# Performance work log

Hardware: AMD Instinct MI355X
Metric: run time of the kernel (lower is better)

The kernel has to match this reference:

```python
import jax, jax.numpy as jnp
import numpy as np

B, N, E, D, H, HW, L = 16, 32, 256, 256, 8, 784, 4
DH = D // H
FF = 4 * D
BN = B * N
BE = B * E
SCALE = 1.0 / np.sqrt(DH)


def _ln(x, g, b):
    m = x.mean(-1, keepdims=True)
    v = ((x - m) ** 2).mean(-1, keepdims=True)
    return (x - m) * jax.lax.rsqrt(v + 1e-5) * g + b


def setup_inputs() -> dict:
    key = jax.random.key(0)
    ks = iter(jax.random.split(key, 64))
    def w(shape, s=0.05):
        return jax.random.normal(next(ks), shape, jnp.float32) * s
    inp = {
        'nodes': w((B, N, D), 1.0),
        'edges': w((B, E, D), 1.0),
        'images': w((B, HW, D), 1.0),
        'mask': jnp.zeros((B * H, N + E, HW), jnp.float32),
        'node_enc': w((BN, D), 1.0),
        'edge_enc': w((BE, D), 1.0),
        'ln1_g': jnp.ones((L, D), jnp.float32), 'ln1_b': jnp.zeros((L, D), jnp.float32),
        'Wqkv': w((L, D, 3 * D)), 'bqkv': jnp.zeros((L, 3 * D), jnp.float32),
        'Wo': w((L, D, D)), 'bo': jnp.zeros((L, D), jnp.float32),
        'ls1': jnp.full((L, D), 0.1, jnp.float32),
        'ln2_g': jnp.ones((L, D), jnp.float32), 'ln2_b': jnp.zeros((L, D), jnp.float32),
        'Wn1': w((L, D, D)), 'bn1': jnp.zeros((L, D), jnp.float32),
        'Wn2': w((L, D, D)), 'bn2': jnp.zeros((L, D), jnp.float32),
        'We': w((L, D, D)), 'be': jnp.zeros((L, D), jnp.float32),
        'attn_p': w((L, H, DH), 1.0),
        'Weo': w((L, D, D)), 'beo': jnp.zeros((L, D), jnp.float32),
        'Wno': w((L, D, D)), 'bno': jnp.zeros((L, D), jnp.float32),
        'ls2': jnp.full((L, D), 0.1, jnp.float32),
        'ln3_g': jnp.ones((L, D), jnp.float32), 'ln3_b': jnp.zeros((L, D), jnp.float32),
        'W1': w((L, D, FF)), 'b1': jnp.zeros((L, FF), jnp.float32),
        'W2': w((L, FF, D)), 'b2': jnp.zeros((L, D), jnp.float32),
        'ls3': jnp.full((L, D), 0.1, jnp.float32),
        'edge_index': jax.random.randint(next(ks), (2, BE), 0, BN, jnp.int32),
    }
    return inp


def reference(nodes, edges, images, mask, node_enc, edge_enc,
              ln1_g, ln1_b, Wqkv, bqkv, Wo, bo, ls1,
              ln2_g, ln2_b, Wn1, bn1, Wn2, bn2, We, be, attn_p, Weo, beo, Wno, bno, ls2,
              ln3_g, ln3_b, W1, b1, W2, b2, ls3, edge_index):
    idx0, idx1 = edge_index[0], edge_index[1]
    ne = jnp.concatenate([nodes, edges], axis=1)  # [B, N+E, D]
    mask4 = mask.reshape(B, H, N + E, HW)
    for l in range(L):
        # cross-attention ne -> images
        ne1n = _ln(ne, ln1_g[l], ln1_b[l])
        q = (ne1n @ Wqkv[l, :, :D] + bqkv[l, :D]).reshape(B, N + E, H, DH)
        k = (images @ Wqkv[l, :, D:2 * D] + bqkv[l, D:2 * D]).reshape(B, HW, H, DH)
        v = (images @ Wqkv[l, :, 2 * D:] + bqkv[l, 2 * D:]).reshape(B, HW, H, DH)
        scores = jnp.einsum('bqhd,bkhd->bhqk', q, k) * SCALE + mask4
        attn = jax.nn.softmax(scores, axis=-1)
        ctx = jnp.einsum('bhqk,bkhd->bqhd', attn, v).reshape(B, N + E, D)
        ne1 = ne + ls1[l] * (ctx @ Wo[l] + bo[l])
        # modified GAT on flattened graph
        ne2n = _ln(ne1, ln2_g[l], ln2_b[l])
        nodes_f = ne2n[:, :N].reshape(BN, D) + node_enc
        edges_f = ne2n[:, N:].reshape(BE, D) + edge_enc
        fn = (nodes_f @ Wn1[l] + bn1[l])[idx0]
        sn = (nodes_f @ Wn2[l] + bn2[l])[idx0]  # NOTE: original code uses edge_index[0] here too
        ep = edges_f @ We[l] + be[l]
        hidden = jax.nn.gelu(fn + sn + ep, approximate=False)  # [BE, D]
        pres = (hidden.reshape(BE, H, DH) * attn_p[l]).sum(-1)  # [BE, H]
        mseg = jax.ops.segment_max(pres, idx0, num_segments=BN)
        expv = jnp.exp(pres - mseg[idx0])
        denom = jax.ops.segment_sum(expv, idx0, num_segments=BN)
        alpha = expv / denom[idx0]  # scatter_softmax over destination nodes
        new_edges = hidden @ Weo[l] + beo[l]
        vals = (nodes_f[idx1] + new_edges) @ Wno[l] + bno[l]
        vals = vals.reshape(BE, H, DH) * alpha[..., None]
        new_nodes = jax.ops.segment_sum(vals.reshape(BE, D), idx0, num_segments=BN)
        gat = jnp.concatenate([new_nodes.reshape(B, N, D), new_edges.reshape(B, E, D)], axis=1)
        ne2 = ne1 + ls2[l] * gat
        # FFN
        ne3n = _ln(ne2, ln3_g[l], ln3_b[l])
        ffn = jax.nn.gelu(ne3n @ W1[l] + b1[l], approximate=False) @ W2[l] + b2[l]
        ne = ne2 + ls3[l] * ffn
    return ne
```

## Files before the change

### kernel.cpp

```cpp
#include <hip/hip_runtime.h>
#include <math.h>

static constexpr int B_  = 16;
static constexpr int N_  = 32;
static constexpr int E_  = 256;
static constexpr int D_  = 256;
static constexpr int H_  = 8;
static constexpr int HW_ = 784;
static constexpr int L_  = 4;
static constexpr int DH_ = 32;
static constexpr int FF_ = 1024;
static constexpr int BN_ = 512;
static constexpr int BE_ = 4096;
static constexpr int NE_ = 288;
static constexpr int NC_ = 13;
static constexpr int NBLK_ = B_ * H_ * 9;
#define SCALE_ 0.17677669529663687f

static constexpr size_t LAYER_W = 1114112;
static constexpr size_t OFF_Q   = 0;
static constexpr size_t OFF_K   = 65536;
static constexpr size_t OFF_WO  = 196608;
static constexpr size_t OFF_WN1 = 262144;
static constexpr size_t OFF_WE  = 393216;
static constexpr size_t OFF_WEO = 458752;
static constexpr size_t OFF_WNO = 524288;
static constexpr size_t OFF_W1  = 589824;
static constexpr size_t OFF_W2  = 851968;

typedef __attribute__((ext_vector_type(8))) short bf16x8;
typedef __attribute__((ext_vector_type(4))) float f32x4;

typedef __attribute__((address_space(1))) const unsigned int gas_uint;
typedef __attribute__((address_space(3))) unsigned int las_uint;

__device__ __forceinline__ void gload16(const unsigned short* g, unsigned short* lds) {
    __builtin_amdgcn_global_load_lds((gas_uint*)g, (las_uint*)lds, 16, 0, 0);
}

__device__ __forceinline__ float gelu_f(float x) {
    return 0.5f * x * (1.0f + erff(x * 0.7071067811865476f));
}

__device__ __forceinline__ unsigned short f2bf(float x) {
    unsigned u = __float_as_uint(x);
    u += 0x7FFFu + ((u >> 16) & 1u);
    return (unsigned short)(u >> 16);
}
__device__ __forceinline__ unsigned pack2bf(float a, float b) {
    return (unsigned)f2bf(a) | ((unsigned)f2bf(b) << 16);
}
__device__ __forceinline__ float bf2f(unsigned short u) {
    return __uint_as_float(((unsigned)u) << 16);
}


__global__ void concat_kernel(const float* __restrict__ nodes, const float* __restrict__ edges,
                              float* __restrict__ ne) {
    int tid = blockIdx.x * 256 + threadIdx.x;
    int d = tid & 255;
    int row = tid >> 8;
    int b = row / NE_, pos = row % NE_;
    float v = (pos < N_) ? nodes[(size_t)(b * N_ + pos) * D_ + d]
                         : edges[(size_t)(b * E_ + (pos - N_)) * D_ + d];
    ne[tid] = v;
}

__global__ void imgcast_kernel(const float* __restrict__ img, unsigned short* __restrict__ out) {
    int tid = blockIdx.x * 256 + threadIdx.x;
    const float* p = img + (size_t)tid * 8;
    float4 a = *(const float4*)(p);
    float4 b = *(const float4*)(p + 4);
    uint4 o = make_uint4(pack2bf(a.x, a.y), pack2bf(a.z, a.w),
                         pack2bf(b.x, b.y), pack2bf(b.z, b.w));
    *(uint4*)&out[(size_t)tid * 8] = o;
}

__global__ void zeroinit_kernel(int* maskflag) {
    if (threadIdx.x == 0 && blockIdx.x == 0) *maskflag = 0;
}

__global__ __launch_bounds__(256) void maskchk_kernel(const float* __restrict__ mask,
                                                      int* __restrict__ flag) {
    const size_t total = (size_t)B_ * H_ * NE_ * HW_ / 4;
    const uint4* m = (const uint4*)mask;
    unsigned acc = 0;
    for (size_t i = (size_t)blockIdx.x * 256 + threadIdx.x; i < total; i += (size_t)gridDim.x * 256) {
        uint4 v = m[i];
        acc |= v.x | v.y | v.z | v.w;
    }
    unsigned long long bal = __ballot(acc != 0);
    if (bal != 0 && (threadIdx.x & 63) == (__ffsll((long long)bal) - 1))
        atomicOr(flag, 1);
}

__global__ __launch_bounds__(128) void premask_kernel(const float* __restrict__ mask,
                                                      unsigned short* __restrict__ pmask,
                                                      const int* __restrict__ flag) {
    if (*flag == 0) return;
    const int bid = blockIdx.x;
    const int c = bid % NC_;
    const int bq = bid / NC_;
    const int h = bq & 7;
    const int qt = (bq >> 3) % 9;
    const int b = (bq >> 3) / 9;
    const int q0 = qt * 32, c0 = c * 64;
    __shared__ float ts[32][68];
    const int t = threadIdx.x;
    const int row = t >> 2, cg = (t & 3) * 16;
    const float* mrow = mask + ((size_t)(b * H_ + h) * NE_ + q0 + row) * (size_t)HW_;
    #pragma unroll
    for (int i = 0; i < 4; ++i) {
        int col = c0 + cg + i * 4;
        float4 m4;
        if (col + 4 <= HW_) {
            m4 = *(const float4*)(mrow + col);
        } else {
            m4.x = (col + 0 < HW_) ? mrow[col + 0] : -1e30f;
            m4.y = (col + 1 < HW_) ? mrow[col + 1] : -1e30f;
            m4.z = (col + 2 < HW_) ? mrow[col + 2] : -1e30f;
            m4.w = (col + 3 < HW_) ? mrow[col + 3] : -1e30f;
        }
        *(float4*)&ts[row][cg + i * 4] = m4;
    }
    __syncthreads();
    const int w = t >> 6, lg = (t & 63) >> 4, lr = t & 15;
    const int r0 = w * 16 + lg * 4;
    unsigned u[8];
    #pragma unroll
    for (int rg = 0; rg < 4; ++rg) {
        u[rg * 2 + 0] = pack2bf(ts[r0 + rg][0 * 16 + lr], ts[r0 + rg][1 * 16 + lr]);
        u[rg * 2 + 1] = pack2bf(ts[r0 + rg][2 * 16 + lr], ts[r0 + rg][3 * 16 + lr]);
    }
    uint4* dst = (uint4*)(pmask + (size_t)bid * 2048 + t * 16);
    dst[0] = make_uint4(u[0], u[1], u[2], u[3]);
    dst[1] = make_uint4(u[4], u[5], u[6], u[7]);
}

__device__ __forceinline__ float ln_from_val(float v, int d,
                                             const float* __restrict__ g, const float* __restrict__ bta,
                                             float* sh1, float* sh2) {
    float s = v, s2 = v * v;
    #pragma unroll
    for (int o = 32; o >= 1; o >>= 1) { s += __shfl_down(s, o); s2 += __shfl_down(s2, o); }
    int lane = d & 63, w = d >> 6;
    if (lane == 0) { sh1[w] = s; sh2[w] = s2; }
    __syncthreads();
    if (d == 0) {
        float a = sh1[0] + sh1[1] + sh1[2] + sh1[3];
        float c = sh2[0] + sh2[1] + sh2[2] + sh2[3];
        sh1[0] = a; sh2[0] = c;
    }
    __syncthreads();
    float mean = sh1[0] * (1.0f / D_);
    float var  = sh2[0] * (1.0f / D_) - mean * mean;
    float rstd = rsqrtf(var + 1e-5f);
    return (v - mean) * rstd * g[d] + bta[d];
}

__global__ __launch_bounds__(256) void ln_kernel(const float* __restrict__ x,
                                                 unsigned short* __restrict__ y,
                                                 const float* __restrict__ g,
                                                 const float* __restrict__ bta) {
    __shared__ float sh1[4], sh2[4];
    const int row = blockIdx.x, d = threadIdx.x;
    float v = x[(size_t)row * D_ + d];
    y[(size_t)row * D_ + d] = f2bf(ln_from_val(v, d, g, bta, sh1, sh2));
}

__global__ __launch_bounds__(256) void ln2enc_kernel(const float* __restrict__ x,
                                                     const float* __restrict__ g,
                                                     const float* __restrict__ bta,
                                                     const float* __restrict__ node_enc,
                                                     const float* __restrict__ edge_enc,
                                                     unsigned short* __restrict__ nodes_f,
                                                     unsigned short* __restrict__ edges_f) {
    __shared__ float sh1[4], sh2[4];
    const int row = blockIdx.x, d = threadIdx.x;
    float v = x[(size_t)row * D_ + d];
    float val = ln_from_val(v, d, g, bta, sh1, sh2);
    int b = row / NE_, pos = row % NE_;
    if (pos < N_) {
        int rn = b * N_ + pos;
        nodes_f[(size_t)rn * D_ + d] = f2bf(val + node_enc[(size_t)rn * D_ + d]);
    } else {
        int re = b * E_ + (pos - N_);
        edges_f[(size_t)re * D_ + d] = f2bf(val + edge_enc[(size_t)re * D_ + d]);
    }
}

__global__ __launch_bounds__(256) void gatagg_ln_kernel(
    const float* __restrict__ vals, const float* __restrict__ pres,
    const int* __restrict__ csr_off, const int* __restrict__ csr_perm,
    const float* __restrict__ new_edges, const float* __restrict__ ls2l,
    const float* __restrict__ g, const float* __restrict__ bta,
    float* __restrict__ ne, unsigned short* __restrict__ lnb) {
    __shared__ float sh1[4], sh2[4];
    __shared__ float sms[8], sden[8];
    const int row = blockIdx.x, d = threadIdx.x;
    int b = row / NE_, pos = row % NE_;
    float gv;
    if (pos < N_) {
        int n = b * N_ + pos;
        int s = csr_off[n], e2 = csr_off[n + 1];
        if (d < 8) {
            float mx = -INFINITY;
            for (int i = s; i < e2; ++i) mx = fmaxf(mx, pres[csr_perm[i] * H_ + d]);
            float sum = 0.f;
            for (int i = s; i < e2; ++i) sum += __expf(pres[csr_perm[i] * H_ + d] - mx);
            sms[d] = mx; sden[d] = sum;
        }
        __syncthreads();
        int h = d >> 5;
        float ms = sms[h];
        float rd = 1.0f / sden[h];
        float acc = 0.f;
        for (int i = s; i < e2; ++i) {
            int e = csr_perm[i];
            acc += vals[(size_t)e * D_ + d] * (__expf(pres[e * H_ + h] - ms) * rd);
        }
        gv = acc;
    } else {
        gv = new_edges[(size_t)(b * E_ + (pos - N_)) * D_ + d];
    }
    float v = ne[(size_t)row * D_ + d] + ls2l[d] * gv;
    ne[(size_t)row * D_ + d] = v;
    lnb[(size_t)row * D_ + d] = f2bf(ln_from_val(v, d, g, bta, sh1, sh2));
}

__global__ __launch_bounds__(256) void wtrans_kernel(
    const float* __restrict__ Wqkv, const float* __restrict__ Wo,
    const float* __restrict__ Wn1,  const float* __restrict__ Wn2,
    const float* __restrict__ We,   const float* __restrict__ Weo,
    const float* __restrict__ Wno,  const float* __restrict__ W1,
    const float* __restrict__ W2,   unsigned short* __restrict__ wT)
{
    const int bid = blockIdx.x;
    const int l = bid / 1088;
    int tl = bid % 1088;
    const float* src; int ld, K, Nn; unsigned short* dst;
    if (tl < 576) {
        int mid = tl >> 6; tl &= 63;
        K = 256; Nn = 256;
        if (mid < 3) {
            src = Wqkv + (size_t)l * 256 * 768 + mid * 256; ld = 768;
            dst = wT + (size_t)l * LAYER_W + (size_t)mid * 65536;
        } else {
            const float* bases[6] = {Wo, Wn1, Wn2, We, Weo, Wno};
            src = bases[mid - 3] + (size_t)l * 65536; ld = 256;
            dst = wT + (size_t)l * LAYER_W + OFF_WO + (size_t)(mid - 3) * 65536;
        }
    } else if (tl < 832) {
        tl -= 576; K = 256; Nn = 1024;
        src = W1 + (size_t)l * 262144; ld = 1024;
        dst = wT + (size_t)l * LAYER_W + OFF_W1;
    } else {
        tl -= 832; K = 1024; Nn = 256;
        src = W2 + (size_t)l * 262144; ld = 256;
        dst = wT + (size_t)l * LAYER_W + OFF_W2;
    }
    const int ntn = Nn >> 5;
    const int k0 = (tl / ntn) << 5, n0 = (tl % ntn) << 5;
    __shared__ float ts[32][33];
    const int t = threadIdx.x;
    const int kl = t >> 5, nl = t & 31;
    #pragma unroll
    for (int rr = 0; rr < 4; ++rr)
        ts[kl + rr * 8][nl] = src[(size_t)(k0 + kl + rr * 8) * ld + n0 + nl];
    __syncthreads();
    const int onl = t >> 3, okl = (t & 7) << 2;
    ushort4 o;
    o.x = f2bf(ts[okl + 0][onl]); o.y = f2bf(ts[okl + 1][onl]);
    o.z = f2bf(ts[okl + 2][onl]); o.w = f2bf(ts[okl + 3][onl]);
    *(ushort4*)&dst[(size_t)(n0 + onl) * K + k0 + okl] = o;
}


struct GArgs {
    const unsigned short* A;
    const unsigned short* Bt;
    const float* bias;
    const float* bias2;
    void* C;
    int lda, ldc, K, outbf, nbx;
};

template<int MODE, int OUTBF>
__global__ __launch_bounds__(256) void mgemm_kernel(
    const unsigned short* __restrict__ A, int lda,
    const unsigned short* __restrict__ Bt,
    const float* __restrict__ bias,
    const float* __restrict__ bias2,
    const float* __restrict__ res,
    const float* __restrict__ ls,
    void* __restrict__ Cv, int ldc, int K)
{
    __shared__ __align__(16) unsigned short As[64 * 64];
    __shared__ __align__(16) unsigned short Bs[64 * 64];
    const int m0 = blockIdx.y * 64, n0 = blockIdx.x * 64;
    const int t = threadIdx.x;
    const int l = t & 63, w = t >> 6;
    const int wr = (w >> 1) * 32, wc = (w & 1) * 32;
    const int frow = l & 15, kg = l >> 4;
    const int srow = w * 8 + (l >> 3);
    const int scolh = 8 * ((l & 7) ^ (l >> 3));
    const int ldsoff = w * 512;
    const int sw = (frow & 7) << 3;
    f32x4 acc[2][2];
    acc[0][0] = (f32x4){0.f,0.f,0.f,0.f}; acc[0][1] = acc[0][0];
    acc[1][0] = acc[0][0];                acc[1][1] = acc[0][0];
    for (int k0 = 0; k0 < K; k0 += 64) {
        const unsigned short* ga = A  + (size_t)(m0 + srow) * lda + k0 + scolh;
        const unsigned short* gb = Bt + (size_t)(n0 + srow) * K   + k0 + scolh;
        gload16(ga,                As + ldsoff);
        gload16(ga + 32 * lda,     As + ldsoff + 2048);
        gload16(gb,                Bs + ldsoff);
        gload16(gb + (size_t)32 * K, Bs + ldsoff + 2048);
        __syncthreads();
        #pragma unroll
        for (int kk = 0; kk < 2; ++kk) {
            const int off = (kk * 32 + kg * 8) ^ sw;
            bf16x8 af0 = *(const bf16x8*)&As[(wr + frow) * 64 + off];
            bf16x8 af1 = *(const bf16x8*)&As[(wr + 16 + frow) * 64 + off];
            bf16x8 bf0 = *(const bf16x8*)&Bs[(wc + frow) * 64 + off];
            bf16x8 bf1 = *(const bf16x8*)&Bs[(wc + 16 + frow) * 64 + off];
            acc[0][0] = __builtin_amdgcn_mfma_f32_16x16x32_bf16(af0, bf0, acc[0][0], 0, 0, 0);
            acc[0][1] = __builtin_amdgcn_mfma_f32_16x16x32_bf16(af0, bf1, acc[0][1], 0, 0, 0);
            acc[1][0] = __builtin_amdgcn_mfma_f32_16x16x32_bf16(af1, bf0, acc[1][0], 0, 0, 0);
            acc[1][1] = __builtin_amdgcn_mfma_f32_16x16x32_bf16(af1, bf1, acc[1][1], 0, 0, 0);
        }
        __syncthreads();
    }
    #pragma unroll
    for (int fr = 0; fr < 2; ++fr) {
        #pragma unroll
        for (int fc = 0; fc < 2; ++fc) {
            int n = n0 + wc + fc * 16 + frow;
            float bv = (bias2 != nullptr && n >= 256) ? bias2[n - 256] : bias[n];
            float lv = (MODE == 2) ? ls[n] : 0.f;
            #pragma unroll
            for (int rg = 0; rg < 4; ++rg) {
                int m = m0 + wr + fr * 16 + kg * 4 + rg;
                float vv = acc[fr][fc][rg] + bv;
                if (MODE == 1) vv = gelu_f(vv);
                if (MODE == 2) vv = res[(size_t)m * ldc + n] + lv * vv;
                if (OUTBF) ((unsigned short*)Cv)[(size_t)m * ldc + n] = f2bf(vv);
                else       ((float*)Cv)[(size_t)m * ldc + n] = vv;
            }
        }
    }
}

__global__ __launch_bounds__(256) void mgemm_weo_kernel(
    const unsigned short* __restrict__ A,
    const unsigned short* __restrict__ Bt,
    const float* __restrict__ bias,
    const unsigned short* __restrict__ nodes_f,
    const int* __restrict__ idx1,
    float* __restrict__ new_edges,
    unsigned short* __restrict__ vin)
{
    __shared__ __align__(16) unsigned short As[64 * 64];
    __shared__ __align__(16) unsigned short Bs[64 * 64];
    const int m0 = blockIdx.y * 64, n0 = blockIdx.x * 64;
    const int t = threadIdx.x;
    const int l = t & 63, w = t >> 6;
    const int wr = (w >> 1) * 32, wc = (w & 1) * 32;
    const int frow = l & 15, kg = l >> 4;
    const int srow = w * 8 + (l >> 3);
    const int scolh = 8 * ((l & 7) ^ (l >> 3));
    const int ldsoff = w * 512;
    const int sw = (frow & 7) << 3;
    f32x4 acc[2][2];
    acc[0][0] = (f32x4){0.f,0.f,0.f,0.f}; acc[0][1] = acc[0][0];
    acc[1][0] = acc[0][0];                acc[1][1] = acc[0][0];
    for (int k0 = 0; k0 < 256; k0 += 64) {
        const unsigned short* ga = A  + (size_t)(m0 + srow) * 256 + k0 + scolh;
        const unsigned short* gb = Bt + (size_t)(n0 + srow) * 256 + k0 + scolh;
        gload16(ga,                 As + ldsoff);
        gload16(ga + 32 * 256,      As + ldsoff + 2048);
        gload16(gb,                 Bs + ldsoff);
        gload16(gb + 32 * 256,      Bs + ldsoff + 2048);
        __syncthreads();
        #pragma unroll
        for (int kk = 0; kk < 2; ++kk) {
            const int off = (kk * 32 + kg * 8) ^ sw;
            bf16x8 af0 = *(const bf16x8*)&As[(wr + frow) * 64 + off];
            bf16x8 af1 = *(const bf16x8*)&As[(wr + 16 + frow) * 64 + off];
            bf16x8 bf0 = *(const bf16x8*)&Bs[(wc + frow) * 64 + off];
            bf16x8 bf1 = *(const bf16x8*)&Bs[(wc + 16 + frow) * 64 + off];
            acc[0][0] = __builtin_amdgcn_mfma_f32_16x16x32_bf16(af0, bf0, acc[0][0], 0, 0, 0);
            acc[0][1] = __builtin_amdgcn_mfma_f32_16x16x32_bf16(af0, bf1, acc[0][1], 0, 0, 0);
            acc[1][0] = __builtin_amdgcn_mfma_f32_16x16x32_bf16(af1, bf0, acc[1][0], 0, 0, 0);
            acc[1][1] = __builtin_amdgcn_mfma_f32_16x16x32_bf16(af1, bf1, acc[1][1], 0, 0, 0);
        }
        __syncthreads();
    }
    #pragma unroll
    for (int fr = 0; fr < 2; ++fr) {
        #pragma unroll
        for (int rg = 0; rg < 4; ++rg) {
            int m = m0 + wr + fr * 16 + kg * 4 + rg;
            int src = idx1[m];
            #pragma unroll
            for (int fc = 0; fc < 2; ++fc) {
                int n = n0 + wc + fc * 16 + frow;
                float vv = acc[fr][fc][rg] + bias[n];
                new_edges[(size_t)m * 256 + n] = vv;
                vin[(size_t)m * 256 + n] = f2bf(bf2f(nodes_f[(size_t)src * 256 + n]) + vv);
            }
        }
    }
}

__global__ __launch_bounds__(256) void mgemm2_kernel(GArgs g0, GArgs g1, int nblk0) {
    const bool first = (int)blockIdx.x < nblk0;
    GArgs g = first ? g0 : g1;
    const int bid = first ? blockIdx.x : blockIdx.x - nblk0;
    __shared__ __align__(16) unsigned short As[64 * 64];
    __shared__ __align__(16) unsigned short Bs[64 * 64];
    const int m0 = (bid / g.nbx) * 64, n0 = (bid % g.nbx) * 64;
    const int t = threadIdx.x;
    const int l = t & 63, w = t >> 6;
    const int wr = (w >> 1) * 32, wc = (w & 1) * 32;
    const int frow = l & 15, kg = l >> 4;
    const int srow = w * 8 + (l >> 3);
    const int scolh = 8 * ((l & 7) ^ (l >> 3));
    const int ldsoff = w * 512;
    const int sw = (frow & 7) << 3;
    f32x4 acc[2][2];
    acc[0][0] = (f32x4){0.f,0.f,0.f,0.f}; acc[0][1] = acc[0][0];
    acc[1][0] = acc[0][0];                acc[1][1] = acc[0][0];
    for (int k0 = 0; k0 < g.K; k0 += 64) {
        const unsigned short* ga = g.A  + (size_t)(m0 + srow) * g.lda + k0 + scolh;
        const unsigned short* gb = g.Bt + (size_t)(n0 + srow) * g.K   + k0 + scolh;
        gload16(ga,                  As + ldsoff);
        gload16(ga + 32 * g.lda,     As + ldsoff + 2048);
        gload16(gb,                  Bs + ldsoff);
        gload16(gb + (size_t)32 * g.K, Bs + ldsoff + 2048);
        __syncthreads();
        #pragma unroll
        for (int kk = 0; kk < 2; ++kk) {
            const int off = (kk * 32 + kg * 8) ^ sw;
            bf16x8 af0 = *(const bf16x8*)&As[(wr + frow) * 64 + off];
            bf16x8 af1 = *(const bf16x8*)&As[(wr + 16 + frow) * 64 + off];
            bf16x8 bf0 = *(const bf16x8*)&Bs[(wc + frow) * 64 + off];
            bf16x8 bf1 = *(const bf16x8*)&Bs[(wc + 16 + frow) * 64 + off];
            acc[0][0] = __builtin_amdgcn_mfma_f32_16x16x32_bf16(af0, bf0, acc[0][0], 0, 0, 0);
            acc[0][1] = __builtin_amdgcn_mfma_f32_16x16x32_bf16(af0, bf1, acc[0][1], 0, 0, 0);
            acc[1][0] = __builtin_amdgcn_mfma_f32_16x16x32_bf16(af1, bf0, acc[1][0], 0, 0, 0);
            acc[1][1] = __builtin_amdgcn_mfma_f32_16x16x32_bf16(af1, bf1, acc[1][1], 0, 0, 0);
        }
        __syncthreads();
    }
    #pragma unroll
    for (int fr = 0; fr < 2; ++fr) {
        #pragma unroll
        for (int fc = 0; fc < 2; ++fc) {
            int n = n0 + wc + fc * 16 + frow;
            float bv = (g.bias2 != nullptr && n >= 256) ? g.bias2[n - 256] : g.bias[n];
            #pragma unroll
            for (int rg = 0; rg < 4; ++rg) {
                int m = m0 + wr + fr * 16 + kg * 4 + rg;
                float vv = acc[fr][fc][rg] + bv;
                if (g.outbf) ((unsigned short*)g.C)[(size_t)m * g.ldc + n] = f2bf(vv);
                else         ((float*)g.C)[(size_t)m * g.ldc + n] = vv;
            }
        }
    }
}

template<int MODE>
__global__ __launch_bounds__(256) void mgemm128_kernel(
    const unsigned short* __restrict__ A, int lda,
    const unsigned short* __restrict__ Bt,
    const float* __restrict__ bias,
    unsigned short* __restrict__ C, int ldc, int K, int nbx)
{
    __shared__ __align__(16) unsigned short As[128 * 64];
    __shared__ __align__(16) unsigned short Bs[128 * 64];
    const int bid = blockIdx.x;
    const int m0 = (bid / nbx) * 128, n0 = (bid % nbx) * 128;
    const int t = threadIdx.x;
    const int l = t & 63, w = t >> 6;
    const int wr = (w >> 1) * 64, wc = (w & 1) * 64;
    const int frow = l & 15, kg = l >> 4;
    const int srow = w * 8 + (l >> 3);
    const int scolh = 8 * ((l & 7) ^ (l >> 3));
    const int ldsoff = w * 512;
    const int sw = (frow & 7) << 3;
    f32x4 acc[4][4];
    #pragma unroll
    for (int i = 0; i < 4; ++i)
        #pragma unroll
        for (int j = 0; j < 4; ++j) acc[i][j] = (f32x4){0.f, 0.f, 0.f, 0.f};
    for (int k0 = 0; k0 < K; k0 += 64) {
        #pragma unroll
        for (int j = 0; j < 4; ++j) {
            gload16(A  + (size_t)(m0 + j * 32 + srow) * lda + k0 + scolh, As + j * 2048 + ldsoff);
            gload16(Bt + (size_t)(n0 + j * 32 + srow) * K   + k0 + scolh, Bs + j * 2048 + ldsoff);
        }
        __syncthreads();
        #pragma unroll
        for (int kk = 0; kk < 2; ++kk) {
            const int off = (kk * 32 + kg * 8) ^ sw;
            bf16x8 af[4], bf[4];
            #pragma unroll
            for (int i = 0; i < 4; ++i) {
                af[i] = *(const bf16x8*)&As[(wr + i * 16 + frow) * 64 + off];
                bf[i] = *(const bf16x8*)&Bs[(wc + i * 16 + frow) * 64 + off];
            }
            #pragma unroll
            for (int i = 0; i < 4; ++i)
                #pragma unroll
                for (int j = 0; j < 4; ++j)
                    acc[i][j] = __builtin_amdgcn_mfma_f32_16x16x32_bf16(af[i], bf[j], acc[i][j], 0, 0, 0);
        }
        __syncthreads();
    }
    #pragma unroll
    for (int fr = 0; fr < 4; ++fr) {
        #pragma unroll
        for (int fc = 0; fc < 4; ++fc) {
            int n = n0 + wc + fc * 16 + frow;
            float bv = bias[n];
            #pragma unroll
            for (int rg = 0; rg < 4; ++rg) {
                int m = m0 + wr + fr * 16 + kg * 4 + rg;
                float vv = acc[fr][fc][rg] + bv;
                if (MODE == 1) vv = gelu_f(vv);
                C[(size_t)m * ldc + n] = f2bf(vv);
            }
        }
    }
}

__global__ __launch_bounds__(128) void attn_kernel(
    const unsigned short* __restrict__ q, const unsigned short* __restrict__ kv,
    const unsigned short* __restrict__ pmask, const int* __restrict__ maskflag,
    unsigned short* __restrict__ ctx)
{
    const int bid = blockIdx.x;
    const int h = bid & 7;
    const int qt = (bid >> 3) % 9;
    const int b = (bid >> 3) / 9;
    const int q0 = qt * 32;
    const int t = threadIdx.x;
    const int w = t >> 6, l = t & 63;
    const int lr = l & 15, lg = l >> 4;
    const int hasmask = *maskflag;

    __shared__ unsigned short Ks[2][64][40];
    __shared__ unsigned short Vs[2][32][72];
    __shared__ unsigned short Pl[2][16][72];

    bf16x8 qfrag = *(const bf16x8*)(q + ((size_t)(b * NE_ + q0 + w * 16 + lr)) * D_ + h * DH_ + lg * 8);

    const int kkey = t >> 1, kdh = (t & 1) * 16;
    const int vdh = (t & 7) * 4, vk0 = (t >> 3) * 2;
    const unsigned short* kbase = kv + ((size_t)b * HW_) * 512 + h * DH_;
    const unsigned short* vbase = kv + ((size_t)b * HW_) * 512 + 256 + h * DH_;
    const uint4* mbase = (const uint4*)(pmask + (size_t)bid * NC_ * 2048 + t * 16);

    uint4 kq0, kq1;
    ushort4 va[2], vb4[2];
    uint4 mc0 = make_uint4(0,0,0,0), mc1 = mc0, mn0 = mc0, mn1 = mc0;

    auto issue_kv = [&](int c0) {
        {
            int key = c0 + kkey;
            bool ok = key < HW_;
            const unsigned short* kp = kbase + (size_t)(ok ? key : 0) * 512 + kdh;
            kq0 = *(const uint4*)(kp);
            kq1 = *(const uint4*)(kp + 8);
            if (!ok) { kq0 = make_uint4(0,0,0,0); kq1 = kq0; }
        }
        #pragma unroll
        for (int r = 0; r < 2; ++r) {
            int key = c0 + vk0 + 32 * r;
            bool ok0 = key < HW_, ok1 = (key + 1) < HW_;
            const unsigned short* vp = vbase + (size_t)(ok0 ? key : 0) * 512 + vdh;
            va[r]  = *(const ushort4*)(vp);
            vb4[r] = *(const ushort4*)(vp + (ok1 ? 512 : 0));
            if (!ok0) va[r]  = make_ushort4(0,0,0,0);
            if (!ok1) vb4[r] = make_ushort4(0,0,0,0);
        }
    };
    auto write_kv = [&](int bufi) {
        *(uint4*)&Ks[bufi][kkey][kdh]     = kq0;
        *(uint4*)&Ks[bufi][kkey][kdh + 8] = kq1;
        #pragma unroll
        for (int r = 0; r < 2; ++r) {
            const unsigned short* a = (const unsigned short*)&va[r];
            const unsigned short* c = (const unsigned short*)&vb4[r];
            #pragma unroll
            for (int i = 0; i < 4; ++i)
                *(unsigned*)&Vs[bufi][vdh + i][vk0 + 32 * r] = (unsigned)a[i] | ((unsigned)c[i] << 16);
        }
    };

    f32x4 oacc[2];
    oacc[0] = (f32x4){0.f, 0.f, 0.f, 0.f}; oacc[1] = oacc[0];
    float m_i[4] = {-INFINITY, -INFINITY, -INFINITY, -INFINITY};
    float l_i[4] = {0.f, 0.f, 0.f, 0.f};

    issue_kv(0);
    if (hasmask) { mc0 = mbase[0]; mc1 = mbase[1]; }
    write_kv(0);
    if (hasmask) { mn0 = mbase[128]; mn1 = mbase[129]; }
    __syncthreads();

    for (int c = 0; c < NC_; ++c) {
        const int c0 = c * 64;
        const int cb = c & 1, nb = cb ^ 1;
        if (c + 1 < NC_) issue_kv(c0 + 64);

        f32x4 sacc[4];
        #pragma unroll
        for (int fc = 0; fc < 4; ++fc) {
            sacc[fc] = (f32x4){0.f, 0.f, 0.f, 0.f};
            bf16x8 kf = *(const bf16x8*)&Ks[cb][fc * 16 + lr][lg * 8];
            sacc[fc] = __builtin_amdgcn_mfma_f32_16x16x32_bf16(qfrag, kf, sacc[fc], 0, 0, 0);
        }
        float s[4][4];
        if (hasmask) {
            unsigned uw[8] = {mc0.x, mc0.y, mc0.z, mc0.w, mc1.x, mc1.y, mc1.z, mc1.w};
            #pragma unroll
            for (int rg = 0; rg < 4; ++rg) {
                s[0][rg] = sacc[0][rg] * SCALE_ + bf2f((unsigned short)(uw[rg * 2] & 0xffff));
                s[1][rg] = sacc[1][rg] * SCALE_ + bf2f((unsigned short)(uw[rg * 2] >> 16));
                s[2][rg] = sacc[2][rg] * SCALE_ + bf2f((unsigned short)(uw[rg * 2 + 1] & 0xffff));
                s[3][rg] = sacc[3][rg] * SCALE_ + bf2f((unsigned short)(uw[rg * 2 + 1] >> 16));
            }
            float mloc[4];
            #pragma unroll
            for (int rg = 0; rg < 4; ++rg)
                mloc[rg] = fmaxf(fmaxf(s[0][rg], s[1][rg]), fmaxf(s[2][rg], s[3][rg]));
            #pragma unroll
            for (int off = 1; off < 16; off <<= 1)
                #pragma unroll
                for (int rg = 0; rg < 4; ++rg)
                    mloc[rg] = fmaxf(mloc[rg], __shfl_xor(mloc[rg], off));
            float scl[4], lloc[4];
            #pragma unroll
            for (int rg = 0; rg < 4; ++rg) {
                float mn = fmaxf(m_i[rg], mloc[rg]);
                scl[rg] = __expf(m_i[rg] - mn);
                m_i[rg] = mn;
            }
            #pragma unroll
            for (int rg = 0; rg < 4; ++rg) {
                float acc = 0.f;
                #pragma unroll
                for (int fc = 0; fc < 4; ++fc) {
                    float p = __expf(s[fc][rg] - m_i[rg]);
                    s[fc][rg] = p;
                    acc += p;
                }
                lloc[rg] = acc;
            }
            #pragma unroll
            for (int off = 1; off < 16; off <<= 1)
                #pragma unroll
                for (int rg = 0; rg < 4; ++rg)
                    lloc[rg] += __shfl_xor(lloc[rg], off);
            #pragma unroll
            for (int rg = 0; rg < 4; ++rg) {
                l_i[rg] = l_i[rg] * scl[rg] + lloc[rg];
                oacc[0][rg] *= scl[rg];
                oacc[1][rg] *= scl[rg];
            }
        } else {
            const bool tailc = (c == NC_ - 1);
            float lloc[4] = {0.f, 0.f, 0.f, 0.f};
            #pragma unroll
            for (int fc = 0; fc < 4; ++fc) {
                float pad = (tailc && (c0 + fc * 16 + lr) >= HW_) ? -1e30f : 0.f;
                #pragma unroll
                for (int rg = 0; rg < 4; ++rg) {
                    float p = __expf(sacc[fc][rg] * SCALE_ + pad);
                    s[fc][rg] = p;
                    lloc[rg] += p;
                }
            }
            #pragma unroll
            for (int off = 1; off < 16; off <<= 1)
                #pragma unroll
                for (int rg = 0; rg < 4; ++rg)
                    lloc[rg] += __shfl_xor(lloc[rg], off);
            #pragma unroll
            for (int rg = 0; rg < 4; ++rg)
                l_i[rg] += lloc[rg];
        }

        #pragma unroll
        for (int fc = 0; fc < 4; ++fc)
            #pragma unroll
            for (int rg = 0; rg < 4; ++rg)
                Pl[w][lg * 4 + rg][fc * 16 + lr] = f2bf(s[fc][rg]);
        #pragma unroll
        for (int ks2 = 0; ks2 < 2; ++ks2) {
            bf16x8 pf = *(const bf16x8*)&Pl[w][lr][ks2 * 32 + lg * 8];
            #pragma unroll
            for (int d2 = 0; d2 < 2; ++d2) {
                bf16x8 vf = *(const bf16x8*)&Vs[cb][d2 * 16 + lr][ks2 * 32 + lg * 8];
                oacc[d2] = __builtin_amdgcn_mfma_f32_16x16x32_bf16(pf, vf, oacc[d2], 0, 0, 0);
            }
        }

        if (hasmask) {
            mc0 = mn0; mc1 = mn1;
            if (c + 2 < NC_) {
                mn0 = mbase[(c + 2) * 128];
                mn1 = mbase[(c + 2) * 128 + 1];
            }
        }
        if (c + 1 < NC_) {
            write_kv(nb);
            __syncthreads();
        }
    }

    unsigned short* cbase = ctx + ((size_t)(b * NE_ + q0 + w * 16 + lg * 4)) * D_ + h * DH_;
    #pragma unroll
    for (int rg = 0; rg < 4; ++rg) {
        float inv = 1.0f / l_i[rg];
        #pragma unroll
        for (int d2 = 0; d2 < 2; ++d2)
            cbase[(size_t)rg * D_ + d2 * 16 + lr] = f2bf(oacc[d2][rg] * inv);
    }
}


__global__ __launch_bounds__(256) void hidden_kernel(
    const float* __restrict__ gn12,
    unsigned short* __restrict__ hid, const int* __restrict__ idx0,
    const float* __restrict__ attn_p_l, float* __restrict__ pres) {
    int e = blockIdx.x;
    int d = threadIdx.x;
    int n = idx0[e];
    float x = bf2f(hid[(size_t)e * D_ + d]) + gn12[(size_t)n * 512 + d] + gn12[(size_t)n * 512 + 256 + d];
    float hv = gelu_f(x);
    hid[(size_t)e * D_ + d] = f2bf(hv);
    float pr = hv * attn_p_l[d];
    #pragma unroll
    for (int o = 1; o < 32; o <<= 1) pr += __shfl_xor(pr, o);
    if ((d & 31) == 0) pres[e * H_ + (d >> 5)] = pr;
}


__global__ __launch_bounds__(512) void csr_build_kernel(const int* __restrict__ idx0,
                                                        int* __restrict__ csr_off) {
    __shared__ int cnt[BN_];
    __shared__ int buf[BN_];
    int t = threadIdx.x;
    cnt[t] = 0;
    __syncthreads();
    #pragma unroll
    for (int i = 0; i < BE_ / 512; ++i)
        atomicAdd(&cnt[idx0[t + i * 512]], 1);
    __syncthreads();
    int c = cnt[t];
    buf[t] = c;
    __syncthreads();
    for (int o = 1; o < BN_; o <<= 1) {
        int add = (t >= o) ? buf[t - o] : 0;
        __syncthreads();
        buf[t] += add;
        __syncthreads();
    }
    csr_off[t] = buf[t] - c;
    if (t == BN_ - 1) csr_off[BN_] = buf[t];
}

__global__ __launch_bounds__(64) void csr_fill(const int* __restrict__ idx0,
                                               const int* __restrict__ csr_off,
                                               int* __restrict__ csr_perm) {
    int n = blockIdx.x;
    int lane = threadIdx.x;
    int w = csr_off[n];
    for (int c0 = 0; c0 < BE_; c0 += 64) {
        int e = c0 + lane;
        bool m = (idx0[e] == n);
        unsigned long long bal = __ballot(m);
        if (m) {
            int pre = __popcll(bal & ((1ull << lane) - 1ull));
            csr_perm[w + pre] = e;
        }
        w += __popcll(bal);
    }
}


static void launch_mgemm(hipStream_t s, int mode, int outbf,
                         const unsigned short* A, int lda, const unsigned short* Bt,
                         const float* bias, const float* bias2, const float* res, const float* ls,
                         void* C, int ldc, int M, int N, int K) {
    dim3 g(N / 64, M / 64);
    if (mode == 0) {
        if (outbf) mgemm_kernel<0,1><<<g, 256, 0, s>>>(A, lda, Bt, bias, bias2, res, ls, C, ldc, K);
        else       mgemm_kernel<0,0><<<g, 256, 0, s>>>(A, lda, Bt, bias, bias2, res, ls, C, ldc, K);
    } else if (mode == 1) {
        mgemm_kernel<1,1><<<g, 256, 0, s>>>(A, lda, Bt, bias, bias2, res, ls, C, ldc, K);
    } else {
        mgemm_kernel<2,0><<<g, 256, 0, s>>>(A, lda, Bt, bias, bias2, res, ls, C, ldc, K);
    }
}

extern "C" void kernel_launch(void* const* d_in, const int* in_sizes, int n_in,
                              void* d_out, int out_size, void* d_ws, size_t ws_size,
                              hipStream_t stream) {
    const float* nodes    = (const float*)d_in[0];
    const float* edges    = (const float*)d_in[1];
    const float* images   = (const float*)d_in[2];
    const float* mask     = (const float*)d_in[3];
    const float* node_enc = (const float*)d_in[4];
    const float* edge_enc = (const float*)d_in[5];
    const float* ln1_g = (const float*)d_in[6];
    const float* ln1_b = (const float*)d_in[7];
    const float* Wqkv  = (const float*)d_in[8];
    const float* bqkv  = (const float*)d_in[9];
    const float* Wo    = (const float*)d_in[10];
    const float* bo    = (const float*)d_in[11];
    const float* ls1   = (const float*)d_in[12];
    const float* ln2_g = (const float*)d_in[13];
    const float* ln2_b = (const float*)d_in[14];
    const float* Wn1   = (const float*)d_in[15];
    const float* bn1   = (const float*)d_in[16];
    const float* Wn2   = (const float*)d_in[17];
    const float* bn2   = (const float*)d_in[18];
    const float* We    = (const float*)d_in[19];
    const float* be    = (const float*)d_in[20];
    const float* attn_p= (const float*)d_in[21];
    const float* Weo   = (const float*)d_in[22];
    const float* beo   = (const float*)d_in[23];
    const float* Wno   = (const float*)d_in[24];
    const float* bno   = (const float*)d_in[25];
    const float* ls2   = (const float*)d_in[26];
    const float* ln3_g = (const float*)d_in[27];
    const float* ln3_b = (const float*)d_in[28];
    const float* W1    = (const float*)d_in[29];
    const float* b1    = (const float*)d_in[30];
    const float* W2    = (const float*)d_in[31];
    const float* b2    = (const float*)d_in[32];
    const float* ls3   = (const float*)d_in[33];
    const int*   edge_index = (const int*)d_in[34];
    const int* idx0 = edge_index;
    const int* idx1 = edge_index + BE_;

    float* ne = (float*)d_out;

    float* cur = (float*)d_ws;
    auto alloc = [&](size_t nfl) { float* p = cur; cur += nfl; return p; };
    auto allocbf = [&](size_t nbf) { float* p = cur; cur += (nbf + 1) / 2; return (unsigned short*)p; };

    unsigned short* lnbuf   = allocbf((size_t)B_ * NE_ * D_);
    unsigned short* qb      = allocbf((size_t)B_ * NE_ * D_);
    unsigned short* kvb     = allocbf((size_t)B_ * HW_ * 512);
    unsigned short* ffnh    = kvb;
    unsigned short* imgbf   = allocbf((size_t)B_ * HW_ * D_);
    unsigned short* ctxb    = allocbf((size_t)B_ * NE_ * D_);
    unsigned short* nodes_f = allocbf((size_t)BN_ * D_);
    unsigned short* edges_f = allocbf((size_t)BE_ * D_);
    unsigned short* hid     = allocbf((size_t)BE_ * D_);
    unsigned short* vin     = allocbf((size_t)BE_ * D_);
    unsigned short* pmaskb  = allocbf((size_t)NBLK_ * NC_ * 2048);
    float* gn12     = alloc((size_t)BN_ * 512);
    float* pres     = alloc((size_t)BE_ * H_);
    float* new_edges= alloc((size_t)BE_ * D_);
    float* valsb    = alloc((size_t)BE_ * D_);
    int* csr_off  = (int*)cur; cur += BN_ + 4;
    int* csr_perm = (int*)cur; cur += BE_;
    int* maskflag = (int*)cur; cur += 4;
    cur = (float*)(((uintptr_t)cur + 255) & ~(uintptr_t)255);
    unsigned short* wT = (unsigned short*)cur;

    zeroinit_kernel<<<1, 64, 0, stream>>>(maskflag);
    maskchk_kernel<<<2048, 256, 0, stream>>>(mask, maskflag);
    wtrans_kernel<<<4 * 1088, 256, 0, stream>>>(Wqkv, Wo, Wn1, Wn2, We, Weo, Wno, W1, W2, wT);
    imgcast_kernel<<<(B_ * HW_ * D_) / (256 * 8), 256, 0, stream>>>(images, imgbf);
    premask_kernel<<<NBLK_ * NC_, 128, 0, stream>>>(mask, pmaskb, maskflag);
    csr_build_kernel<<<1, 512, 0, stream>>>(idx0, csr_off);
    csr_fill<<<BN_, 64, 0, stream>>>(idx0, csr_off, csr_perm);
    concat_kernel<<<(B_ * NE_ * D_) / 256, 256, 0, stream>>>(nodes, edges, ne);

    for (int l = 0; l < L_; ++l) {
        const unsigned short* wTl = wT + (size_t)l * LAYER_W;
        const float* bqkv_l = bqkv + (size_t)l * 3 * D_;

        ln_kernel<<<B_ * NE_, 256, 0, stream>>>(ne, lnbuf, ln1_g + l * D_, ln1_b + l * D_);
        {
            GArgs gq { lnbuf, wTl + OFF_Q, bqkv_l, nullptr, qb, 256, 256, 256, 1, 4 };
            GArgs gkv{ imgbf, wTl + OFF_K, bqkv_l + D_, nullptr, kvb, 256, 512, 256, 1, 8 };
            int nb0 = (B_ * NE_ / 64) * 4;
            int nb1 = (B_ * HW_ / 64) * 8;
            mgemm2_kernel<<<nb0 + nb1, 256, 0, stream>>>(gq, gkv, nb0);
        }
        attn_kernel<<<NBLK_, 128, 0, stream>>>(qb, kvb, pmaskb, maskflag, ctxb);
        launch_mgemm(stream, 2, 0, ctxb, D_, wTl + OFF_WO, bo + l * D_, nullptr, ne, ls1 + l * D_,
                     ne, D_, B_ * NE_, D_, D_);

        ln2enc_kernel<<<B_ * NE_, 256, 0, stream>>>(ne, ln2_g + l * D_, ln2_b + l * D_,
                                                    node_enc, edge_enc, nodes_f, edges_f);
        {
            GArgs gn { nodes_f, wTl + OFF_WN1, bn1 + l * D_, bn2 + l * D_, gn12, 256, 512, 256, 0, 8 };
            GArgs ge { edges_f, wTl + OFF_WE,  be + l * D_,  nullptr,      hid,  256, 256, 256, 1, 4 };
            int nb0 = (BN_ / 64) * 8;
            int nb1 = (BE_ / 64) * 4;
            mgemm2_kernel<<<nb0 + nb1, 256, 0, stream>>>(gn, ge, nb0);
        }
        hidden_kernel<<<BE_, 256, 0, stream>>>(gn12, hid, idx0, attn_p + (size_t)l * H_ * DH_, pres);
        mgemm_weo_kernel<<<dim3(4, BE_ / 64), 256, 0, stream>>>(
            hid, wTl + OFF_WEO, beo + l * D_, nodes_f, idx1, new_edges, vin);
        launch_mgemm(stream, 0, 0, vin, D_, wTl + OFF_WNO, bno + l * D_, nullptr, nullptr, nullptr,
                     valsb, D_, BE_, D_, D_);
        gatagg_ln_kernel<<<B_ * NE_, 256, 0, stream>>>(valsb, pres, csr_off, csr_perm,
                                                       new_edges, ls2 + l * D_,
                                                       ln3_g + l * D_, ln3_b + l * D_, ne, lnbuf);

        mgemm128_kernel<1><<<(B_ * NE_ / 128) * (FF_ / 128), 256, 0, stream>>>(
            lnbuf, 256, wTl + OFF_W1, b1 + l * FF_, ffnh, FF_, 256, FF_ / 128);
        launch_mgemm(stream, 2, 0, ffnh, FF_, wTl + OFF_W2, b2 + l * D_, nullptr, ne, ls3 + l * D_,
                     ne, D_, B_ * NE_, D_, FF_);
    }
}
```

Measured before the change: 589.9 us.

## Hoist K/V projections for all layers into one GEMM; fuse Q projection into attention

The K/V projection of the images does not depend on the layer input, so all four layers' K/V projections are computed up front in a single larger 128x128-tile GEMM writing a per-layer KV buffer. The Q projection is folded into the attention kernel: each block loads its 32 LN rows and the head's 32 weight rows into LDS, computes Q with MFMA and stages it through LDS to form the query fragment. This removes one GEMM launch per layer and the Q round-trip through global memory. In exchange it needs a larger KV buffer, and each attention block recomputes Q for its own tile, reusing the K staging LDS.

```diff
diff --git a/kernel.cpp b/kernel.cpp
--- a/kernel.cpp
+++ b/kernel.cpp
@@ -15,11 +15,11 @@
 static constexpr int NE_ = 288;
 static constexpr int NC_ = 13;
 static constexpr int NBLK_ = B_ * H_ * 9;
+static constexpr size_t KVSZ_ = (size_t)B_ * HW_ * 512;
 #define SCALE_ 0.17677669529663687f
 
 static constexpr size_t LAYER_W = 1114112;
 static constexpr size_t OFF_Q   = 0;
-static constexpr size_t OFF_K   = 65536;
 static constexpr size_t OFF_WO  = 196608;
 static constexpr size_t OFF_WN1 = 262144;
 static constexpr size_t OFF_WE  = 393216;
@@ -233,7 +233,8 @@
     const float* __restrict__ Wn1,  const float* __restrict__ Wn2,
     const float* __restrict__ We,   const float* __restrict__ Weo,
     const float* __restrict__ Wno,  const float* __restrict__ W1,
-    const float* __restrict__ W2,   unsigned short* __restrict__ wT)
+    const float* __restrict__ W2,   unsigned short* __restrict__ wT,
+    unsigned short* __restrict__ kvwT)
 {
     const int bid = blockIdx.x;
     const int l = bid / 1088;
@@ -242,9 +243,12 @@
     if (tl < 576) {
         int mid = tl >> 6; tl &= 63;
         K = 256; Nn = 256;
-        if (mid < 3) {
+        if (mid == 0) {
+            src = Wqkv + (size_t)l * 256 * 768; ld = 768;
+            dst = wT + (size_t)l * LAYER_W + OFF_Q;
+        } else if (mid < 3) {
             src = Wqkv + (size_t)l * 256 * 768 + mid * 256; ld = 768;
-            dst = wT + (size_t)l * LAYER_W + (size_t)mid * 65536;
+            dst = kvwT + ((size_t)l * 512 + (size_t)(mid - 1) * 256) * 256;
         } else {
             const float* bases[6] = {Wo, Wn1, Wn2, We, Weo, Wno};
             src = bases[mid - 3] + (size_t)l * 65536; ld = 256;
@@ -535,8 +539,74 @@
     }
 }
 
+__global__ __launch_bounds__(256) void mgemmkv_kernel(
+    const unsigned short* __restrict__ A,
+    const unsigned short* __restrict__ kvwT,
+    const float* __restrict__ bqkv,
+    unsigned short* __restrict__ kvall)
+{
+    __shared__ __align__(16) unsigned short As[128 * 64];
+    __shared__ __align__(16) unsigned short Bs[128 * 64];
+    const int bid = blockIdx.x;
+    const int m0 = (bid / 16) * 128, n0 = (bid % 16) * 128;
+    const int t = threadIdx.x;
+    const int l = t & 63, w = t >> 6;
+    const int wr = (w >> 1) * 64, wc = (w & 1) * 64;
+    const int frow = l & 15, kg = l >> 4;
+    const int srow = w * 8 + (l >> 3);
+    const int scolh = 8 * ((l & 7) ^ (l >> 3));
+    const int ldsoff = w * 512;
+    const int sw = (frow & 7) << 3;
+    f32x4 acc[4][4];
+    #pragma unroll
+    for (int i = 0; i < 4; ++i)
+        #pragma unroll
+        for (int j = 0; j < 4; ++j) acc[i][j] = (f32x4){0.f, 0.f, 0.f, 0.f};
+    for (int k0 = 0; k0 < 256; k0 += 64) {
+        #pragma unroll
+        for (int j = 0; j < 4; ++j) {
+            gload16(A    + (size_t)(m0 + j * 32 + srow) * 256 + k0 + scolh, As + j * 2048 + ldsoff);
+            gload16(kvwT + (size_t)(n0 + j * 32 + srow) * 256 + k0 + scolh, Bs + j * 2048 + ldsoff);
+        }
+        __syncthreads();
+        #pragma unroll
+        for (int kk = 0; kk < 2; ++kk) {
+            const int off = (kk * 32 + kg * 8) ^ sw;
+            bf16x8 af[4], bf[4];
+            #pragma unroll
+            for (int i = 0; i < 4; ++i) {
+                af[i] = *(const bf16x8*)&As[(wr + i * 16 + frow) * 64 + off];
+                bf[i] = *(const bf16x8*)&Bs[(wc + i * 16 + frow) * 64 + off];
+            }
+            #pragma unroll
+            for (int i = 0; i < 4; ++i)
+                #pragma unroll
+                for (int j = 0; j < 4; ++j)
+                    acc[i][j] = __builtin_amdgcn_mfma_f32_16x16x32_bf16(af[i], bf[j], acc[i][j], 0, 0, 0);
+        }
+        __syncthreads();
+    }
+    #pragma unroll
+    for (int fr = 0; fr < 4; ++fr) {
+        #pragma unroll
+        for (int fc = 0; fc < 4; ++fc) {
+            int n = n0 + wc + fc * 16 + frow;
+            int layer = n >> 9, nn = n & 511;
+            float bv = bqkv[layer * 768 + 256 + nn];
+            unsigned short* dst = kvall + (size_t)layer * KVSZ_ + nn;
+            #pragma unroll
+            for (int rg = 0; rg < 4; ++rg) {
+                int m = m0 + wr + fr * 16 + kg * 4 + rg;
+                dst[(size_t)m * 512] = f2bf(acc[fr][fc][rg] + bv);
+            }
+        }
+    }
+}
+
 __global__ __launch_bounds__(128) void attn_kernel(
-    const unsigned short* __restrict__ q, const unsigned short* __restrict__ kv,
+    const unsigned short* __restrict__ lnb, const unsigned short* __restrict__ wq,
+    const float* __restrict__ bqkv_l,
+    const unsigned short* __restrict__ kv,
     const unsigned short* __restrict__ pmask, const int* __restrict__ maskflag,
     unsigned short* __restrict__ ctx)
 {
@@ -553,8 +623,7 @@
     __shared__ unsigned short Ks[2][64][40];
     __shared__ unsigned short Vs[2][32][72];
     __shared__ unsigned short Pl[2][16][72];
-
-    bf16x8 qfrag = *(const bf16x8*)(q + ((size_t)(b * NE_ + q0 + w * 16 + lr)) * D_ + h * DH_ + lg * 8);
+    __shared__ unsigned short Qlds[2][16][40];
 
     const int kkey = t >> 1, kdh = (t & 1) * 16;
     const int vdh = (t & 7) * 4, vk0 = (t >> 3) * 2;
@@ -599,13 +668,51 @@
         }
     };
 
+    issue_kv(0);
+    if (hasmask) { mc0 = mbase[0]; mc1 = mbase[1]; }
+
+    bf16x8 qfrag;
+    {
+        unsigned short* Aln = &Ks[0][0][0];
+        unsigned short* Wqs = Aln + 32 * 264;
+        const unsigned short* asrc = lnb + (size_t)(b * NE_ + q0) * 256;
+        const unsigned short* wsrc = wq + (size_t)(h * DH_) * 256;
+        #pragma unroll
+        for (int i = 0; i < 8; ++i) {
+            int u = t + i * 128;
+            int row = u >> 5, col = (u & 31) * 8;
+            *(uint4*)&Aln[row * 264 + col] = *(const uint4*)&asrc[(size_t)row * 256 + col];
+            *(uint4*)&Wqs[row * 264 + col] = *(const uint4*)&wsrc[(size_t)row * 256 + col];
+        }
+        __syncthreads();
+        f32x4 qa[2];
+        qa[0] = (f32x4){0.f, 0.f, 0.f, 0.f}; qa[1] = qa[0];
+        #pragma unroll
+        for (int kk = 0; kk < 8; ++kk) {
+            bf16x8 af = *(const bf16x8*)&Aln[(w * 16 + lr) * 264 + kk * 32 + lg * 8];
+            #pragma unroll
+            for (int fc = 0; fc < 2; ++fc) {
+                bf16x8 bf = *(const bf16x8*)&Wqs[(fc * 16 + lr) * 264 + kk * 32 + lg * 8];
+                qa[fc] = __builtin_amdgcn_mfma_f32_16x16x32_bf16(af, bf, qa[fc], 0, 0, 0);
+            }
+        }
+        __syncthreads();
+        #pragma unroll
+        for (int fc = 0; fc < 2; ++fc) {
+            float bq = bqkv_l[h * DH_ + fc * 16 + lr];
+            #pragma unroll
+            for (int rg = 0; rg < 4; ++rg)
+                Qlds[w][lg * 4 + rg][fc * 16 + lr] = f2bf(qa[fc][rg] + bq);
+        }
+        __syncthreads();
+        qfrag = *(const bf16x8*)&Qlds[w][lr][lg * 8];
+    }
+
     f32x4 oacc[2];
     oacc[0] = (f32x4){0.f, 0.f, 0.f, 0.f}; oacc[1] = oacc[0];
     float m_i[4] = {-INFINITY, -INFINITY, -INFINITY, -INFINITY};
     float l_i[4] = {0.f, 0.f, 0.f, 0.f};
 
-    issue_kv(0);
-    if (hasmask) { mc0 = mbase[0]; mc1 = mbase[1]; }
     write_kv(0);
     if (hasmask) { mn0 = mbase[128]; mn1 = mbase[129]; }
     __syncthreads();
@@ -855,9 +962,8 @@
     auto allocbf = [&](size_t nbf) { float* p = cur; cur += (nbf + 1) / 2; return (unsigned short*)p; };
 
     unsigned short* lnbuf   = allocbf((size_t)B_ * NE_ * D_);
-    unsigned short* qb      = allocbf((size_t)B_ * NE_ * D_);
-    unsigned short* kvb     = allocbf((size_t)B_ * HW_ * 512);
-    unsigned short* ffnh    = kvb;
+    unsigned short* kvall   = allocbf((size_t)L_ * KVSZ_);
+    unsigned short* ffnh    = allocbf((size_t)B_ * NE_ * FF_);
     unsigned short* imgbf   = allocbf((size_t)B_ * HW_ * D_);
     unsigned short* ctxb    = allocbf((size_t)B_ * NE_ * D_);
     unsigned short* nodes_f = allocbf((size_t)BN_ * D_);
@@ -865,6 +971,7 @@
     unsigned short* hid     = allocbf((size_t)BE_ * D_);
     unsigned short* vin     = allocbf((size_t)BE_ * D_);
     unsigned short* pmaskb  = allocbf((size_t)NBLK_ * NC_ * 2048);
+    unsigned short* kvwT    = allocbf((size_t)L_ * 512 * 256);
     float* gn12     = alloc((size_t)BN_ * 512);
     float* pres     = alloc((size_t)BE_ * H_);
     float* new_edges= alloc((size_t)BE_ * D_);
@@ -877,26 +984,21 @@
 
     zeroinit_kernel<<<1, 64, 0, stream>>>(maskflag);
     maskchk_kernel<<<2048, 256, 0, stream>>>(mask, maskflag);
-    wtrans_kernel<<<4 * 1088, 256, 0, stream>>>(Wqkv, Wo, Wn1, Wn2, We, Weo, Wno, W1, W2, wT);
+    wtrans_kernel<<<4 * 1088, 256, 0, stream>>>(Wqkv, Wo, Wn1, Wn2, We, Weo, Wno, W1, W2, wT, kvwT);
     imgcast_kernel<<<(B_ * HW_ * D_) / (256 * 8), 256, 0, stream>>>(images, imgbf);
     premask_kernel<<<NBLK_ * NC_, 128, 0, stream>>>(mask, pmaskb, maskflag);
     csr_build_kernel<<<1, 512, 0, stream>>>(idx0, csr_off);
     csr_fill<<<BN_, 64, 0, stream>>>(idx0, csr_off, csr_perm);
     concat_kernel<<<(B_ * NE_ * D_) / 256, 256, 0, stream>>>(nodes, edges, ne);
+    mgemmkv_kernel<<<(B_ * HW_ / 128) * 16, 256, 0, stream>>>(imgbf, kvwT, bqkv, kvall);
 
     for (int l = 0; l < L_; ++l) {
         const unsigned short* wTl = wT + (size_t)l * LAYER_W;
         const float* bqkv_l = bqkv + (size_t)l * 3 * D_;
 
         ln_kernel<<<B_ * NE_, 256, 0, stream>>>(ne, lnbuf, ln1_g + l * D_, ln1_b + l * D_);
-        {
-            GArgs gq { lnbuf, wTl + OFF_Q, bqkv_l, nullptr, qb, 256, 256, 256, 1, 4 };
-            GArgs gkv{ imgbf, wTl + OFF_K, bqkv_l + D_, nullptr, kvb, 256, 512, 256, 1, 8 };
-            int nb0 = (B_ * NE_ / 64) * 4;
-            int nb1 = (B_ * HW_ / 64) * 8;
-            mgemm2_kernel<<<nb0 + nb1, 256, 0, stream>>>(gq, gkv, nb0);
-        }
-        attn_kernel<<<NBLK_, 128, 0, stream>>>(qb, kvb, pmaskb, maskflag, ctxb);
+        attn_kernel<<<NBLK_, 128, 0, stream>>>(lnbuf, wTl + OFF_Q, bqkv_l,
+                                               kvall + (size_t)l * KVSZ_, pmaskb, maskflag, ctxb);
         launch_mgemm(stream, 2, 0, ctxb, D_, wTl + OFF_WO, bo + l * D_, nullptr, ne, ls1 + l * D_,
                      ne, D_, B_ * NE_, D_, D_);
 
```

Measured after the change: 589.0 us. No clear change (-0.2%).
